# Performance work log

Measured on AMD Instinct MI355X. Metric: run time of the kernel, lower is better.

## Reference

```python
import jax, jax.numpy as jnp
import numpy as np

N_NODES, N_EDGES, NUM_GRAPHS = 50000, 800000, 64
F_DIM, H_DIM, N_LAYERS, N_CLASSES = 64, 64, 3, 16
EPS = 1e-5  # StdAggregation epsilon (PyG)


def setup_inputs() -> dict:
    key = jax.random.key(0)
    ks = jax.random.split(key, 12)
    s = 0.05
    x = jax.random.normal(ks[0], (N_NODES, F_DIM), jnp.float32)
    edge_index = jax.random.randint(ks[1], (2, N_EDGES), 0, N_NODES, dtype=jnp.int32)
    batch = jnp.sort(jax.random.randint(ks[2], (N_NODES,), 0, NUM_GRAPHS, dtype=jnp.int32))
    # per-layer PNAConv params (towers=1): pre Linear(2F->F), post Linear(13F->H), lin Linear(H->H)
    pre_w = jax.random.normal(ks[3], (N_LAYERS, F_DIM, 2 * F_DIM), jnp.float32) * s
    pre_b = jnp.zeros((N_LAYERS, F_DIM), jnp.float32)
    post_w = jax.random.normal(ks[4], (N_LAYERS, H_DIM, 13 * F_DIM), jnp.float32) * s
    post_b = jnp.zeros((N_LAYERS, H_DIM), jnp.float32)
    lin_w = jax.random.normal(ks[5], (N_LAYERS, H_DIM, H_DIM), jnp.float32) * s
    lin_b = jnp.zeros((N_LAYERS, H_DIM), jnp.float32)
    mlp_w1 = jax.random.normal(ks[6], (H_DIM, H_DIM), jnp.float32) * s
    mlp_b1 = jnp.zeros((H_DIM,), jnp.float32)
    mlp_w2 = jax.random.normal(ks[7], (N_CLASSES, H_DIM), jnp.float32) * s
    mlp_b2 = jnp.zeros((N_CLASSES,), jnp.float32)
    return dict(x=x, edge_index=edge_index, batch=batch,
                pre_w=pre_w, pre_b=pre_b, post_w=post_w, post_b=post_b,
                lin_w=lin_w, lin_b=lin_b, mlp_w1=mlp_w1, mlp_b1=mlp_b1,
                mlp_w2=mlp_w2, mlp_b2=mlp_b2)


def pna_forward(x, src, dst, pre_w, pre_b, post_w, post_b, lin_w, lin_b,
                mlp_w1, mlp_b1, mlp_w2, mlp_b2, batch):
    N = x.shape[0]
    deg_raw = jax.ops.segment_sum(jnp.ones_like(src, jnp.float32), dst, N)  # in-degree [N]
    deg = jnp.maximum(deg_raw, 1.0)[:, None]
    # avg log degree (PNA avg_deg['log'] from the degree histogram of this graph)
    avg_log = jnp.mean(jnp.log(deg_raw + 1.0))
    log_deg = jnp.log(deg + 1.0)
    amp = log_deg / avg_log          # amplification scaler [N,1]
    att = avg_log / log_deg          # attenuation scaler [N,1]
    has_in = (deg_raw > 0)[:, None]

    for l in range(pre_w.shape[0]):
        h = jnp.concatenate([x[dst], x[src]], axis=-1)        # [E, 2F] (x_i, x_j)
        m = h @ pre_w[l].T + pre_b[l]                          # pre_nn message [E, F]
        s1 = jax.ops.segment_sum(m, dst, N)
        s2 = jax.ops.segment_sum(m * m, dst, N)
        mean = s1 / deg
        std = jnp.sqrt(jax.nn.relu(s2 / deg - mean * mean) + EPS)
        mn = jnp.where(has_in, jax.ops.segment_min(m, dst, N), 0.0)
        mx = jnp.where(has_in, jax.ops.segment_max(m, dst, N), 0.0)
        aggr = jnp.concatenate([mean, mn, mx, std], axis=-1)   # [N, 4F]
        out = jnp.concatenate([x, aggr, aggr * amp, aggr * att], axis=-1)  # [N, 13F]
        out = out @ post_w[l].T + post_b[l]                    # post_nn [N, H]
        x = jax.nn.relu(out @ lin_w[l].T + lin_b[l])           # conv.lin + outer ReLU

    # global mean pool over graphs
    counts = jnp.maximum(
        jax.ops.segment_sum(jnp.ones((N,), x.dtype), batch, NUM_GRAPHS), 1.0)
    g = jax.ops.segment_sum(x, batch, NUM_GRAPHS) / counts[:, None]  # [G, H]
    g = jax.nn.relu(g @ mlp_w1.T + mlp_b1)
    return g @ mlp_w2.T + mlp_b2                               # [G, C]


def reference(x, edge_index, batch, pre_w, pre_b, post_w, post_b,
              lin_w, lin_b, mlp_w1, mlp_b1, mlp_w2, mlp_b2):
    src, dst = edge_index[0], edge_index[1]
    return pna_forward(x, src, dst, pre_w, pre_b, post_w, post_b,
                       lin_w, lin_b, mlp_w1, mlp_b1, mlp_w2, mlp_b2, batch)
```

## Files before the change

kernel.cpp:

```cpp
#include <hip/hip_runtime.h>
#include <math.h>

#define N_NODES   50000
#define N_EDGES   800000
#define NUM_GRAPHS 64
#define FDIM      64
#define HDIM      64
#define NLAYERS   3
#define NCLASSES  16
#define EPS       1e-5f

#define SCAN_CHUNK 1024
#define NCHUNKS ((N_NODES + SCAN_CHUNK - 1) / SCAN_CHUNK)

typedef unsigned short u16;
typedef unsigned int   u32;
typedef __attribute__((ext_vector_type(8))) short short8;
typedef __attribute__((ext_vector_type(4))) float floatx4;

#define WKS_LAYER 159744
#define PRES_LAYER 24576
#define KPOST_LDS_BYTES 106496

__device__ inline void split1(float f, u16& h, u16& m, u16& l) {
    u32 b  = __float_as_uint(f);
    u32 hb = b & 0xFFFF0000u;
    float r = f - __uint_as_float(hb);
    u32 mb = __float_as_uint(r) & 0xFFFF0000u;
    float r2 = r - __uint_as_float(mb);
    u32 lb = __float_as_uint(r2) & 0xFFFF0000u;
    h = (u16)(hb >> 16); m = (u16)(mb >> 16); l = (u16)(lb >> 16);
}

__device__ inline void gl_lds16(const void* g, void* l) {
    __builtin_amdgcn_global_load_lds(
        (const __attribute__((address_space(1))) u32*)g,
        (__attribute__((address_space(3))) u32*)l, 16, 0, 0);
}

__global__ __launch_bounds__(256) void k_comb(const float* __restrict__ post_w,
                                              const float* __restrict__ lin_w,
                                              const float* __restrict__ pre_w,
                                              const float* __restrict__ post_b,
                                              const float* __restrict__ lin_b,
                                              u16* __restrict__ WkS,
                                              u16* __restrict__ PreS,
                                              float* __restrict__ bcv,
                                              int* __restrict__ cnt,
                                              float* __restrict__ logsum) {
    int b = blockIdx.x, t = threadIdx.x;
    int zi = b * 256 + t;
    if (zi < N_NODES) cnt[zi] = 0;
    if (zi == 0) *logsum = 0.f;

    if (b < 624) {
        int c  = t & 63;
        int kl = t >> 6;
        int l  = b / 208;
        int o  = (b % 208) * 4 + kl;
        const float* lw = lin_w + (size_t)l * 4096 + c * 64;
        const float* pw = post_w + (size_t)l * 53248 + o;
        float acc = 0.f;
        #pragma unroll 8
        for (int j = 0; j < 64; ++j)
            acc += lw[j] * pw[(size_t)j * 832];
        u16 h, m, lo;
        split1(acc, h, m, lo);

        int kn;
        if (o < 64) kn = o;
        else {
            int s  = (o - 64) >> 8;
            int mm = (o - 64) & 255;
            int j  = mm >> 5, r = mm & 31;
            kn = 64 + j * 96 + s * 32 + r;
        }
        int ch  = kn >> 5;
        int kin = kn & 31;
        int n16 = c & 15, nt = c >> 4;
        int swk = (((kin >> 3) + (n16 >> 1)) & 3) * 8 + (kin & 7);
        size_t base = (size_t)l * WKS_LAYER + (size_t)ch * 6144
                    + nt * 512 + n16 * 32 + swk;
        WkS[base]        = h;
        WkS[base + 2048] = m;
        WkS[base + 4096] = lo;
    } else if (b == 624) {
        if (t < 192) {
            int l = t >> 6, c = t & 63;
            float acc = lin_b[l * 64 + c];
            for (int j = 0; j < 64; ++j)
                acc += lin_w[(size_t)l * 4096 + c * 64 + j] * post_b[l * 64 + j];
            bcv[l * 64 + c] = acc;
        }
    } else {
        int i = (b - 625) * 256 + t;
        int l = i >> 13;
        int rem = i & 8191;
        int c128 = rem >> 6;
        int k = rem & 63;
        float v;
        if (c128 < 64) v = pre_w[(size_t)l * 8192 + c128 * 128 + k];
        else           v = pre_w[(size_t)l * 8192 + (c128 - 64) * 128 + 64 + k];
        u16 h, m, lo;
        split1(v, h, m, lo);
        int ch = k >> 5, kin = k & 31;
        int nt = c128 >> 4, n16 = c128 & 15;
        int swk = (((kin >> 3) + (n16 >> 1)) & 3) * 8 + (kin & 7);
        size_t base = (size_t)l * PRES_LAYER + (size_t)ch * 12288
                    + nt * 512 + n16 * 32 + swk;
        PreS[base]        = h;
        PreS[base + 4096] = m;
        PreS[base + 8192] = lo;
    }
}

__global__ void k_count(const int* __restrict__ dst, int* __restrict__ cnt,
                        int* __restrict__ rank) {
    int e = blockIdx.x * 256 + threadIdx.x;
    if (e < N_EDGES) rank[e] = atomicAdd(&cnt[dst[e]], 1);
}

__global__ void k_chunk_sums(const int* __restrict__ cnt, int* __restrict__ bsum,
                             float* __restrict__ logsum) {
    __shared__ int   ired[256];
    __shared__ float lred[256];
    int b = blockIdx.x, t = threadIdx.x;
    int base = b * SCAN_CHUNK;
    int s = 0; float ls = 0.f;
    for (int i = t; i < SCAN_CHUNK; i += 256) {
        int idx = base + i;
        if (idx < N_NODES) {
            int v = cnt[idx];
            s += v;
            ls += logf((float)v + 1.0f);
        }
    }
    ired[t] = s; lred[t] = ls;
    __syncthreads();
    for (int off = 128; off > 0; off >>= 1) {
        if (t < off) { ired[t] += ired[t + off]; lred[t] += lred[t + off]; }
        __syncthreads();
    }
    if (t == 0) { bsum[b] = ired[0]; atomicAdd(logsum, lred[0]); }
}

__global__ void k_scan_top(const int* __restrict__ bsum, int* __restrict__ boff,
                           int* __restrict__ row_start) {
    if (threadIdx.x == 0) {
        int acc = 0;
        for (int i = 0; i < NCHUNKS; ++i) { boff[i] = acc; acc += bsum[i]; }
        row_start[N_NODES] = acc;
    }
}

__global__ void k_scan_chunks(const int* __restrict__ cnt, const int* __restrict__ boff,
                              int* __restrict__ row_start) {
    __shared__ int tsum[256];
    int b = blockIdx.x, t = threadIdx.x;
    int base = b * SCAN_CHUNK + t * 4;
    int v[4]; int s = 0;
    #pragma unroll
    for (int i = 0; i < 4; ++i) {
        int idx = base + i;
        v[i] = (idx < N_NODES) ? cnt[idx] : 0;
        s += v[i];
    }
    tsum[t] = s;
    __syncthreads();
    for (int off = 1; off < 256; off <<= 1) {
        int val = (t >= off) ? tsum[t - off] : 0;
        __syncthreads();
        tsum[t] += val;
        __syncthreads();
    }
    int excl = boff[b] + tsum[t] - s;
    #pragma unroll
    for (int i = 0; i < 4; ++i) {
        int idx = base + i;
        if (idx < N_NODES) row_start[idx] = excl;
        excl += v[i];
    }
}

__global__ void k_scatter(const int* __restrict__ src, const int* __restrict__ dst,
                          const int* __restrict__ rank,
                          const int* __restrict__ row_start,
                          int* __restrict__ csr_src) {
    int e = blockIdx.x * 256 + threadIdx.x;
    if (e < N_EDGES) {
        int d = dst[e];
        csr_src[row_start[d] + rank[e]] = src[e];
    }
}

__global__ void k_scal(const int* __restrict__ cnt, const float* __restrict__ logsum,
                       float* __restrict__ inv_deg, float* __restrict__ ampv,
                       float* __restrict__ attv, float* __restrict__ g_sum,
                       int* __restrict__ g_cnt) {
    int n = blockIdx.x * 256 + threadIdx.x;
    if (blockIdx.x == 0) {
        for (int i = threadIdx.x; i < 4096; i += 256) g_sum[i] = 0.f;
        if (threadIdx.x < 64) g_cnt[threadIdx.x] = 0;
    }
    if (n < N_NODES) {
        float avg = logsum[0] / (float)N_NODES;
        float degf = fmaxf((float)cnt[n], 1.0f);
        inv_deg[n] = 1.0f / degf;
        float ld = logf(degf + 1.0f);
        ampv[n] = ld / avg;
        attv[n] = avg / ld;
    }
}

__global__ __launch_bounds__(256, 4) void k_pre(const float* __restrict__ x,
                                                const u16* __restrict__ PreS,
                                                const float* __restrict__ pre_b,
                                                float* __restrict__ p,
                                                float* __restrict__ q) {
    __shared__ u16 ldsB[2 * 8192];
    int t = threadIdx.x;
    int w = t >> 6;
    int lane = t & 63;
    int m = lane & 15;
    int qh = lane >> 4;
    int rowBase = blockIdx.x * 64;

    int myrow = rowBase + 16 * w + m;
    bool vr = myrow < N_NODES;
    int crow = vr ? myrow : 0;
    const float* xrow = x + (size_t)crow * 64;

    int bo = m * 32 + ((qh + (m >> 1)) & 3) * 8;

    for (int u = w; u < 32; u += 4) {
        int ch = u >> 4, sp = (u >> 3) & 1, nt = u & 7;
        const char* g = (const char*)PreS + (size_t)ch * 24576 + sp * 8192
                      + nt * 1024 + lane * 16;
        char* l = (char*)ldsB + u * 1024;
        gl_lds16(g, l);
    }
    float fa[2][8];
    #pragma unroll
    for (int ch = 0; ch < 2; ++ch) {
        const float* sp = xrow + ch * 32 + qh * 8;
        float4 u0 = *(const float4*)sp;
        float4 u1 = *(const float4*)(sp + 4);
        fa[ch][0] = vr ? u0.x : 0.f; fa[ch][1] = vr ? u0.y : 0.f;
        fa[ch][2] = vr ? u0.z : 0.f; fa[ch][3] = vr ? u0.w : 0.f;
        fa[ch][4] = vr ? u1.x : 0.f; fa[ch][5] = vr ? u1.y : 0.f;
        fa[ch][6] = vr ? u1.z : 0.f; fa[ch][7] = vr ? u1.w : 0.f;
    }
    asm volatile("s_waitcnt vmcnt(0)" ::: "memory");
    __syncthreads();

    floatx4 acc[8] = {};
    #pragma unroll
    for (int ch = 0; ch < 2; ++ch) {
        union { u32 u[4]; short8 s8; } AH, AM;
        #pragma unroll
        for (int i = 0; i < 4; ++i) {
            float f0 = fa[ch][2 * i], f1 = fa[ch][2 * i + 1];
            u32 b0 = __float_as_uint(f0), b1 = __float_as_uint(f1);
            u32 h0 = b0 & 0xFFFF0000u,  h1 = b1 & 0xFFFF0000u;
            float r0 = f0 - __uint_as_float(h0);
            float r1 = f1 - __uint_as_float(h1);
            u32 m0 = __float_as_uint(r0) & 0xFFFF0000u;
            u32 m1 = __float_as_uint(r1) & 0xFFFF0000u;
            AH.u[i] = (h0 >> 16) | h1;
            AM.u[i] = (m0 >> 16) | m1;
        }
        const u16* Bb = ldsB + ch * 8192;
        #pragma unroll
        for (int nt = 0; nt < 8; ++nt) {
            short8 bH = *(const short8*)(Bb + nt * 512 + bo);
            short8 bM = *(const short8*)(Bb + 4096 + nt * 512 + bo);
            acc[nt] = __builtin_amdgcn_mfma_f32_16x16x32_bf16(AH.s8, bH, acc[nt], 0, 0, 0);
            acc[nt] = __builtin_amdgcn_mfma_f32_16x16x32_bf16(AH.s8, bM, acc[nt], 0, 0, 0);
            acc[nt] = __builtin_amdgcn_mfma_f32_16x16x32_bf16(AM.s8, bH, acc[nt], 0, 0, 0);
        }
    }

    int col = m;
    #pragma unroll
    for (int nt = 0; nt < 8; ++nt) {
        int cbase = (nt & 3) * 16 + col;
        float bias = (nt < 4) ? pre_b[cbase] : 0.f;
        float* outp = (nt < 4) ? p : q;
        #pragma unroll
        for (int reg = 0; reg < 4; ++reg) {
            int grow = rowBase + 16 * w + qh * 4 + reg;
            if (grow < N_NODES)
                outp[(size_t)grow * 64 + cbase] = acc[nt][reg] + bias;
        }
    }
}

__global__ __launch_bounds__(256) void k_aggr(const float* __restrict__ p,
                                              const float* __restrict__ q,
                                              const int* __restrict__ row_start,
                                              const int* __restrict__ csr_src,
                                              const float* __restrict__ inv_deg,
                                              float* __restrict__ aggr) {
    int wid  = (blockIdx.x * 256 + threadIdx.x) >> 6;
    int lane = threadIdx.x & 63;
    if (wid >= N_NODES) return;
    int n = wid;
    int beg = row_start[n], end = row_start[n + 1];
    float sum = 0.f, sq = 0.f;
    float mn = INFINITY, mx = -INFINITY;
    int e = beg;
    for (; e + 7 < end; e += 8) {
        float qv[8];
        #pragma unroll
        for (int u = 0; u < 8; ++u) {
            int s = csr_src[e + u];
            qv[u] = q[(size_t)s * 64 + lane];
        }
        #pragma unroll
        for (int u = 0; u < 8; ++u) {
            float m = qv[u];
            sum += m; sq += m * m;
            mn = fminf(mn, m); mx = fmaxf(mx, m);
        }
    }
    for (; e + 3 < end; e += 4) {
        float qv[4];
        #pragma unroll
        for (int u = 0; u < 4; ++u) {
            int s = csr_src[e + u];
            qv[u] = q[(size_t)s * 64 + lane];
        }
        #pragma unroll
        for (int u = 0; u < 4; ++u) {
            float m = qv[u];
            sum += m; sq += m * m;
            mn = fminf(mn, m); mx = fmaxf(mx, m);
        }
    }
    for (; e < end; ++e) {
        int s = csr_src[e];
        float m = q[(size_t)s * 64 + lane];
        sum += m; sq += m * m;
        mn = fminf(mn, m); mx = fmaxf(mx, m);
    }
    float* a = aggr + (size_t)n * 256;
    if (end <= beg) {
        a[lane]       = 0.f;
        a[64 + lane]  = 0.f;
        a[128 + lane] = 0.f;
        a[192 + lane] = sqrtf(EPS);
    } else {
        float pv = p[n * 64 + lane];
        float id = inv_deg[n];
        float meanq = sum * id;
        float var = fmaxf(sq * id - meanq * meanq, 0.f);
        a[lane]       = pv + meanq;
        a[64 + lane]  = pv + mn;
        a[128 + lane] = pv + mx;
        a[192 + lane] = sqrtf(var + EPS);
    }
}

__global__ __launch_bounds__(1024, 4) void k_post(const float* __restrict__ x,
                                                  const float* __restrict__ aggr,
                                                  const float* __restrict__ ampv,
                                                  const float* __restrict__ attv,
                                                  const u16* __restrict__ WkS,
                                                  const float* __restrict__ bc,
                                                  float* __restrict__ xout) {
    extern __shared__ u16 ldsB[];
    int t = threadIdx.x;
    int w = t >> 6;
    int lane = t & 63;
    int m = lane & 15;
    int qh = lane >> 4;

    int b  = blockIdx.x;
    int s8 = b & 7;
    int g  = b >> 3;
    int q2 = g >> 1;
    int nh = g & 1;
    int r  = 8 * q2 + s8;
    if (r >= 98) return;
    int rowBase = r * 512 + 32 * w;

    for (int u = w; u < 104; u += 16) {
        int ch = u >> 2;
        int sp = (u >> 1) & 1;
        int h2 = u & 1;
        const char* gp = (const char*)WkS + ch * 12288 + sp * 4096
                       + nh * 2048 + h2 * 1024 + lane * 16;
        char* l = (char*)ldsB + u * 1024;
        gl_lds16(gp, l);
    }

    int row0 = rowBase + m;
    int row1 = row0 + 16;
    int cr0 = (row0 < N_NODES) ? row0 : 0;
    int cr1 = (row1 < N_NODES) ? row1 : 0;
    const float* xr0 = x + (size_t)cr0 * 64;
    const float* xr1 = x + (size_t)cr1 * 64;
    const float* ar0 = aggr + (size_t)cr0 * 256;
    const float* ar1 = aggr + (size_t)cr1 * 256;

    int bo = m * 32 + ((qh + (m >> 1)) & 3) * 8;

    floatx4 accP0[2] = {}, accA0[2] = {}, accT0[2] = {};
    floatx4 accP1[2] = {}, accA1[2] = {}, accT1[2] = {};

    float f0[8], f1[8];
    union U8 { u32 u[4]; short8 s8v; };
    U8 AH0, AM0, AH1, AM1;

    auto loadRaw = [&](const float* sp, float* f) {
        float4 u0 = *(const float4*)(sp + qh * 8);
        float4 u1 = *(const float4*)(sp + qh * 8 + 4);
        f[0] = u0.x; f[1] = u0.y; f[2] = u0.z; f[3] = u0.w;
        f[4] = u1.x; f[5] = u1.y; f[6] = u1.z; f[7] = u1.w;
    };
    auto split2 = [&](const float* f, U8& H, U8& M8) {
        #pragma unroll
        for (int i = 0; i < 4; ++i) {
            float v0 = f[2 * i], v1 = f[2 * i + 1];
            u32 b0 = __float_as_uint(v0), b1 = __float_as_uint(v1);
            u32 h0 = b0 & 0xFFFF0000u,  h1 = b1 & 0xFFFF0000u;
            float r0 = v0 - __uint_as_float(h0);
            float r1 = v1 - __uint_as_float(h1);
            u32 m0 = __float_as_uint(r0) & 0xFFFF0000u;
            u32 m1 = __float_as_uint(r1) & 0xFFFF0000u;
            H.u[i]  = (h0 >> 16) | h1;
            M8.u[i] = (m0 >> 16) | m1;
        }
    };
    #define MF(A, B, C) C = __builtin_amdgcn_mfma_f32_16x16x32_bf16((A).s8v, (B), (C), 0, 0, 0)
    auto chunkMM = [&](int ch, floatx4* A0, floatx4* A1) {
        const u16* pB = ldsB + ch * 2048 + bo;
        short8 bH0 = *(const short8*)(pB);
        short8 bH1 = *(const short8*)(pB + 512);
        short8 bM0 = *(const short8*)(pB + 1024);
        short8 bM1 = *(const short8*)(pB + 1536);
        MF(AH0, bH0, A0[0]); MF(AH1, bH0, A1[0]); MF(AH0, bH1, A0[1]); MF(AH1, bH1, A1[1]);
        MF(AH0, bM0, A0[0]); MF(AH1, bM0, A1[0]); MF(AH0, bM1, A0[1]); MF(AH1, bM1, A1[1]);
        MF(AM0, bH0, A0[0]); MF(AM1, bH0, A1[0]); MF(AM0, bH1, A0[1]); MF(AM1, bH1, A1[1]);
    };

    loadRaw(xr0, f0); loadRaw(xr1, f1);
    asm volatile("s_waitcnt vmcnt(0)" ::: "memory");
    __syncthreads();

    split2(f0, AH0, AM0); split2(f1, AH1, AM1);
    loadRaw(xr0 + 32, f0); loadRaw(xr1 + 32, f1);
    chunkMM(0, accP0, accP1);
    split2(f0, AH0, AM0); split2(f1, AH1, AM1);
    loadRaw(ar0, f0); loadRaw(ar1, f1);
    chunkMM(1, accP0, accP1);
    for (int j = 0; j < 8; ++j) {
        split2(f0, AH0, AM0); split2(f1, AH1, AM1);
        if (j < 7) { loadRaw(ar0 + (j + 1) * 32, f0); loadRaw(ar1 + (j + 1) * 32, f1); }
        int ch = 2 + 3 * j;
        chunkMM(ch,     accP0, accP1);
        chunkMM(ch + 1, accA0, accA1);
        chunkMM(ch + 2, accT0, accT1);
    }
    #undef MF

    int col = m;
    #pragma unroll
    for (int frag = 0; frag < 2; ++frag) {
        #pragma unroll
        for (int reg = 0; reg < 4; ++reg) {
            int grow = rowBase + 16 * frag + qh * 4 + reg;
            if (grow < N_NODES) {
                float av = ampv[grow], tv = attv[grow];
                #pragma unroll
                for (int nt = 0; nt < 2; ++nt) {
                    int cbase = (nh * 2 + nt) * 16 + col;
                    float pv  = frag ? accP1[nt][reg] : accP0[nt][reg];
                    float av2 = frag ? accA1[nt][reg] : accA0[nt][reg];
                    float tv2 = frag ? accT1[nt][reg] : accT0[nt][reg];
                    float v = pv + av * av2 + tv * tv2 + bc[cbase];
                    xout[(size_t)grow * 64 + cbase] = fmaxf(v, 0.f);
                }
            }
        }
    }
}

__global__ __launch_bounds__(256) void k_pool(const float* __restrict__ x,
                                              const int* __restrict__ batch,
                                              float* __restrict__ g_sum,
                                              int* __restrict__ g_cnt) {
    int lane = threadIdx.x & 63;
    int wave = blockIdx.x * 4 + (threadIdx.x >> 6);
    const int NPW = 16;
    int beg = wave * NPW;
    if (beg >= N_NODES) return;
    int end = min(beg + NPW, N_NODES);
    float acc = 0.f;
    int cur = batch[beg];
    int c = 0;
    for (int n = beg; n < end; ++n) {
        int b = batch[n];
        if (b != cur) {
            atomicAdd(&g_sum[cur * 64 + lane], acc);
            if (lane == 0) atomicAdd(&g_cnt[cur], c);
            acc = 0.f; c = 0; cur = b;
        }
        acc += x[n * 64 + lane];
        ++c;
    }
    atomicAdd(&g_sum[cur * 64 + lane], acc);
    if (lane == 0) atomicAdd(&g_cnt[cur], c);
}

__global__ __launch_bounds__(256) void k_mlp(const float* __restrict__ g_sum,
                                             const int* __restrict__ g_cnt,
                                             const float* __restrict__ w1,
                                             const float* __restrict__ b1,
                                             const float* __restrict__ w2,
                                             const float* __restrict__ b2,
                                             float* __restrict__ out) {
    __shared__ float g[64][64];
    __shared__ float h[64][64];
    __shared__ float wT[64][65];
    int t = threadIdx.x;
    for (int idx = t; idx < 4096; idx += 256) {
        int gi = idx >> 6, c = idx & 63;
        float cntf = fmaxf((float)g_cnt[gi], 1.f);
        g[gi][c] = g_sum[idx] / cntf;
    }
    for (int idx = t; idx < 4096; idx += 256) {
        int c = idx >> 6, k = idx & 63;
        wT[k][c] = w1[c * 64 + k];
    }
    __syncthreads();
    for (int idx = t; idx < 4096; idx += 256) {
        int gi = idx >> 6, c = idx & 63;
        float acc = b1[c];
        for (int k = 0; k < 64; ++k) acc += g[gi][k] * wT[k][c];
        h[gi][c] = fmaxf(acc, 0.f);
    }
    __syncthreads();
    for (int idx = t; idx < 64 * NCLASSES; idx += 256) {
        int gi = idx >> 4, c = idx & 15;
        float acc = b2[c];
        for (int k = 0; k < 64; ++k) acc += h[gi][k] * w2[c * 64 + k];
        out[gi * NCLASSES + c] = acc;
    }
}

extern "C" void kernel_launch(void* const* d_in, const int* in_sizes, int n_in,
                              void* d_out, int out_size, void* d_ws, size_t ws_size,
                              hipStream_t stream) {
    const float* x      = (const float*)d_in[0];
    const int*   ei     = (const int*)d_in[1];
    const int*   batch  = (const int*)d_in[2];
    const float* pre_w  = (const float*)d_in[3];
    const float* pre_b  = (const float*)d_in[4];
    const float* post_w = (const float*)d_in[5];
    const float* post_b = (const float*)d_in[6];
    const float* lin_w  = (const float*)d_in[7];
    const float* lin_b  = (const float*)d_in[8];
    const float* mlp_w1 = (const float*)d_in[9];
    const float* mlp_b1 = (const float*)d_in[10];
    const float* mlp_w2 = (const float*)d_in[11];
    const float* mlp_b2 = (const float*)d_in[12];

    const int* src = ei;
    const int* dst = ei + N_EDGES;

    char* base = (char*)d_ws;
    size_t off = 0;
    auto alloc = [&](size_t bytes) -> void* {
        void* ptr = base + off;
        off += (bytes + 255) & ~(size_t)255;
        return ptr;
    };
    int*   cnt       = (int*)alloc(N_NODES * 4);
    int*   row_start = (int*)alloc((N_NODES + 1) * 4);
    int*   rank      = (int*)alloc(N_EDGES * 4);
    int*   csr_src   = (int*)alloc(N_EDGES * 4);
    int*   bsum      = (int*)alloc(64 * 4);
    int*   boff      = (int*)alloc(64 * 4);
    float* logsum    = (float*)alloc(16);
    float* inv_deg   = (float*)alloc(N_NODES * 4);
    float* ampv      = (float*)alloc(N_NODES * 4);
    float* attv      = (float*)alloc(N_NODES * 4);
    float* p         = (float*)alloc((size_t)N_NODES * 64 * 4);
    float* q         = (float*)alloc((size_t)N_NODES * 64 * 4);
    float* aggr      = (float*)alloc((size_t)N_NODES * 256 * 4);
    float* xb0       = (float*)alloc((size_t)N_NODES * 64 * 4);
    float* xb1       = (float*)alloc((size_t)N_NODES * 64 * 4);
    float* g_sum     = (float*)alloc(64 * 64 * 4);
    int*   g_cnt     = (int*)alloc(64 * 4);
    u16*   WkS       = (u16*)alloc((size_t)3 * WKS_LAYER * 2);
    u16*   PreS      = (u16*)alloc((size_t)3 * PRES_LAYER * 2);
    float* bcv       = (float*)alloc(3 * 64 * 4);

    k_comb<<<721, 256, 0, stream>>>(post_w, lin_w, pre_w, post_b, lin_b,
                                    WkS, PreS, bcv, cnt, logsum);

    k_count<<<(N_EDGES + 255) / 256, 256, 0, stream>>>(dst, cnt, rank);
    k_chunk_sums<<<NCHUNKS, 256, 0, stream>>>(cnt, bsum, logsum);
    k_scan_top<<<1, 64, 0, stream>>>(bsum, boff, row_start);
    k_scan_chunks<<<NCHUNKS, 256, 0, stream>>>(cnt, boff, row_start);
    k_scatter<<<(N_EDGES + 255) / 256, 256, 0, stream>>>(src, dst, rank,
                                                         row_start, csr_src);
    k_scal<<<(N_NODES + 255) / 256, 256, 0, stream>>>(cnt, logsum, inv_deg,
                                                      ampv, attv, g_sum, g_cnt);

    const int PRE_BLOCKS  = (N_NODES + 63) / 64;
    const int POST_BLOCKS = 208;
    const float* xin = x;
    float* bufs[3] = {xb0, xb1, xb0};
    for (int l = 0; l < NLAYERS; ++l) {
        k_pre<<<PRE_BLOCKS, 256, 0, stream>>>(xin, PreS + (size_t)l * PRES_LAYER,
                                              pre_b + l * 64, p, q);
        k_aggr<<<(N_NODES + 3) / 4, 256, 0, stream>>>(p, q, row_start, csr_src,
                                                      inv_deg, aggr);
        float* xo = bufs[l];
        k_post<<<POST_BLOCKS, 1024, KPOST_LDS_BYTES, stream>>>(
            xin, aggr, ampv, attv, WkS + (size_t)l * WKS_LAYER,
            bcv + l * 64, xo);
        xin = xo;
    }

    int pool_waves = (N_NODES + 15) / 16;
    k_pool<<<(pool_waves + 3) / 4, 256, 0, stream>>>(xin, batch, g_sum, g_cnt);
    k_mlp<<<1, 256, 0, stream>>>(g_sum, g_cnt, mlp_w1, mlp_b1, mlp_w2, mlp_b2,
                                 (float*)d_out);
}
```

Baseline: 408.2 us.

## Fuse degree scalars and scan top into scan kernel; fuse pooling into last post

```diff
diff --git a/kernel.cpp b/kernel.cpp
--- a/kernel.cpp
+++ b/kernel.cpp
@@ -47,11 +47,15 @@
                                               u16* __restrict__ PreS,
                                               float* __restrict__ bcv,
                                               int* __restrict__ cnt,
-                                              float* __restrict__ logsum) {
+                                              float* __restrict__ logsum,
+                                              float* __restrict__ g_sum,
+                                              int* __restrict__ g_cnt) {
     int b = blockIdx.x, t = threadIdx.x;
     int zi = b * 256 + t;
     if (zi < N_NODES) cnt[zi] = 0;
     if (zi == 0) *logsum = 0.f;
+    if (zi < 4096) g_sum[zi] = 0.f;
+    if (zi < 64)   g_cnt[zi] = 0;
 
     if (b < 624) {
         int c  = t & 63;
@@ -144,19 +148,21 @@
     if (t == 0) { bsum[b] = ired[0]; atomicAdd(logsum, lred[0]); }
 }
 
-__global__ void k_scan_top(const int* __restrict__ bsum, int* __restrict__ boff,
-                           int* __restrict__ row_start) {
-    if (threadIdx.x == 0) {
-        int acc = 0;
-        for (int i = 0; i < NCHUNKS; ++i) { boff[i] = acc; acc += bsum[i]; }
-        row_start[N_NODES] = acc;
-    }
-}
-
-__global__ void k_scan_chunks(const int* __restrict__ cnt, const int* __restrict__ boff,
-                              int* __restrict__ row_start) {
+__global__ __launch_bounds__(256) void k_scan2(const int* __restrict__ cnt,
+                                               const int* __restrict__ bsum,
+                                               const float* __restrict__ logsum,
+                                               const int* __restrict__ batch,
+                                               int* __restrict__ row_start,
+                                               float* __restrict__ inv_deg,
+                                               float* __restrict__ ampv,
+                                               float* __restrict__ attv,
+                                               int* __restrict__ g_cnt) {
     __shared__ int tsum[256];
     int b = blockIdx.x, t = threadIdx.x;
+
+    int boffb = 0;
+    for (int i = 0; i < b; ++i) boffb += bsum[i];
+
     int base = b * SCAN_CHUNK + t * 4;
     int v[4]; int s = 0;
     #pragma unroll
@@ -173,13 +179,31 @@
         tsum[t] += val;
         __syncthreads();
     }
-    int excl = boff[b] + tsum[t] - s;
+    int excl = boffb + tsum[t] - s;
+    float avg = logsum[0] / (float)N_NODES;
+
+    int curb = -1, c = 0;
     #pragma unroll
     for (int i = 0; i < 4; ++i) {
         int idx = base + i;
-        if (idx < N_NODES) row_start[idx] = excl;
-        excl += v[i];
-    }
+        if (idx < N_NODES) {
+            row_start[idx] = excl;
+            excl += v[i];
+            float degf = fmaxf((float)v[i], 1.0f);
+            inv_deg[idx] = 1.0f / degf;
+            float ld = logf(degf + 1.0f);
+            ampv[idx] = ld / avg;
+            attv[idx] = avg / ld;
+            int bb = batch[idx];
+            if (bb != curb) {
+                if (c) atomicAdd(&g_cnt[curb], c);
+                curb = bb; c = 0;
+            }
+            ++c;
+        }
+    }
+    if (c) atomicAdd(&g_cnt[curb], c);
+    if (b == 0 && t == 0) row_start[N_NODES] = N_EDGES;
 }
 
 __global__ void k_scatter(const int* __restrict__ src, const int* __restrict__ dst,
@@ -190,25 +214,6 @@
     if (e < N_EDGES) {
         int d = dst[e];
         csr_src[row_start[d] + rank[e]] = src[e];
-    }
-}
-
-__global__ void k_scal(const int* __restrict__ cnt, const float* __restrict__ logsum,
-                       float* __restrict__ inv_deg, float* __restrict__ ampv,
-                       float* __restrict__ attv, float* __restrict__ g_sum,
-                       int* __restrict__ g_cnt) {
-    int n = blockIdx.x * 256 + threadIdx.x;
-    if (blockIdx.x == 0) {
-        for (int i = threadIdx.x; i < 4096; i += 256) g_sum[i] = 0.f;
-        if (threadIdx.x < 64) g_cnt[threadIdx.x] = 0;
-    }
-    if (n < N_NODES) {
-        float avg = logsum[0] / (float)N_NODES;
-        float degf = fmaxf((float)cnt[n], 1.0f);
-        inv_deg[n] = 1.0f / degf;
-        float ld = logf(degf + 1.0f);
-        ampv[n] = ld / avg;
-        attv[n] = avg / ld;
     }
 }
 
@@ -367,7 +372,9 @@
                                                   const float* __restrict__ attv,
                                                   const u16* __restrict__ WkS,
                                                   const float* __restrict__ bc,
-                                                  float* __restrict__ xout) {
+                                                  float* __restrict__ xout,
+                                                  const int* __restrict__ batch,
+                                                  float* __restrict__ g_sum) {
     extern __shared__ u16 ldsB[];
     int t = threadIdx.x;
     int w = t >> 6;
@@ -465,52 +472,64 @@
     #undef MF
 
     int col = m;
-    #pragma unroll
-    for (int frag = 0; frag < 2; ++frag) {
-        #pragma unroll
-        for (int reg = 0; reg < 4; ++reg) {
-            int grow = rowBase + 16 * frag + qh * 4 + reg;
-            if (grow < N_NODES) {
-                float av = ampv[grow], tv = attv[grow];
-                #pragma unroll
-                for (int nt = 0; nt < 2; ++nt) {
-                    int cbase = (nh * 2 + nt) * 16 + col;
-                    float pv  = frag ? accP1[nt][reg] : accP0[nt][reg];
-                    float av2 = frag ? accA1[nt][reg] : accA0[nt][reg];
-                    float tv2 = frag ? accT1[nt][reg] : accT0[nt][reg];
-                    float v = pv + av * av2 + tv * tv2 + bc[cbase];
-                    xout[(size_t)grow * 64 + cbase] = fmaxf(v, 0.f);
+    int cb0 = (nh * 2 + 0) * 16 + col;
+    int cb1 = (nh * 2 + 1) * 16 + col;
+    if (batch == nullptr) {
+        #pragma unroll
+        for (int frag = 0; frag < 2; ++frag) {
+            #pragma unroll
+            for (int reg = 0; reg < 4; ++reg) {
+                int grow = rowBase + 16 * frag + qh * 4 + reg;
+                if (grow < N_NODES) {
+                    float av = ampv[grow], tv = attv[grow];
+                    #pragma unroll
+                    for (int nt = 0; nt < 2; ++nt) {
+                        int cbase = nt ? cb1 : cb0;
+                        float pv  = frag ? accP1[nt][reg] : accP0[nt][reg];
+                        float av2 = frag ? accA1[nt][reg] : accA0[nt][reg];
+                        float tv2 = frag ? accT1[nt][reg] : accT0[nt][reg];
+                        float v = pv + av * av2 + tv * tv2 + bc[cbase];
+                        xout[(size_t)grow * 64 + cbase] = fmaxf(v, 0.f);
+                    }
                 }
             }
         }
-    }
-}
-
-__global__ __launch_bounds__(256) void k_pool(const float* __restrict__ x,
-                                              const int* __restrict__ batch,
-                                              float* __restrict__ g_sum,
-                                              int* __restrict__ g_cnt) {
-    int lane = threadIdx.x & 63;
-    int wave = blockIdx.x * 4 + (threadIdx.x >> 6);
-    const int NPW = 16;
-    int beg = wave * NPW;
-    if (beg >= N_NODES) return;
-    int end = min(beg + NPW, N_NODES);
-    float acc = 0.f;
-    int cur = batch[beg];
-    int c = 0;
-    for (int n = beg; n < end; ++n) {
-        int b = batch[n];
-        if (b != cur) {
-            atomicAdd(&g_sum[cur * 64 + lane], acc);
-            if (lane == 0) atomicAdd(&g_cnt[cur], c);
-            acc = 0.f; c = 0; cur = b;
-        }
-        acc += x[n * 64 + lane];
-        ++c;
-    }
-    atomicAdd(&g_sum[cur * 64 + lane], acc);
-    if (lane == 0) atomicAdd(&g_cnt[cur], c);
+    } else {
+        float acc0 = 0.f, acc1 = 0.f;
+        int cur = -1;
+        float bias0 = bc[cb0], bias1 = bc[cb1];
+        #pragma unroll
+        for (int frag = 0; frag < 2; ++frag) {
+            #pragma unroll
+            for (int reg = 0; reg < 4; ++reg) {
+                int grow = rowBase + 16 * frag + qh * 4 + reg;
+                if (grow < N_NODES) {
+                    float av = ampv[grow], tv = attv[grow];
+                    float p0 = frag ? accP0[0][reg] * 0.f + accP1[0][reg] : accP0[0][reg];
+                    float a0 = frag ? accA1[0][reg] : accA0[0][reg];
+                    float t0 = frag ? accT1[0][reg] : accT0[0][reg];
+                    float p1 = frag ? accP1[1][reg] : accP0[1][reg];
+                    float a1 = frag ? accA1[1][reg] : accA0[1][reg];
+                    float t1 = frag ? accT1[1][reg] : accT0[1][reg];
+                    float v0 = fmaxf(p0 + av * a0 + tv * t0 + bias0, 0.f);
+                    float v1 = fmaxf(p1 + av * a1 + tv * t1 + bias1, 0.f);
+                    int bb = batch[grow];
+                    if (bb != cur) {
+                        if (cur >= 0) {
+                            atomicAdd(&g_sum[cur * 64 + cb0], acc0);
+                            atomicAdd(&g_sum[cur * 64 + cb1], acc1);
+                        }
+                        cur = bb; acc0 = 0.f; acc1 = 0.f;
+                    }
+                    acc0 += v0; acc1 += v1;
+                }
+            }
+        }
+        if (cur >= 0) {
+            atomicAdd(&g_sum[cur * 64 + cb0], acc0);
+            atomicAdd(&g_sum[cur * 64 + cb1], acc1);
+        }
+    }
 }
 
 __global__ __launch_bounds__(256) void k_mlp(const float* __restrict__ g_sum,
@@ -581,7 +600,6 @@
     int*   rank      = (int*)alloc(N_EDGES * 4);
     int*   csr_src   = (int*)alloc(N_EDGES * 4);
     int*   bsum      = (int*)alloc(64 * 4);
-    int*   boff      = (int*)alloc(64 * 4);
     float* logsum    = (float*)alloc(16);
     float* inv_deg   = (float*)alloc(N_NODES * 4);
     float* ampv      = (float*)alloc(N_NODES * 4);
@@ -598,16 +616,14 @@
     float* bcv       = (float*)alloc(3 * 64 * 4);
 
     k_comb<<<721, 256, 0, stream>>>(post_w, lin_w, pre_w, post_b, lin_b,
-                                    WkS, PreS, bcv, cnt, logsum);
+                                    WkS, PreS, bcv, cnt, logsum, g_sum, g_cnt);
 
     k_count<<<(N_EDGES + 255) / 256, 256, 0, stream>>>(dst, cnt, rank);
     k_chunk_sums<<<NCHUNKS, 256, 0, stream>>>(cnt, bsum, logsum);
-    k_scan_top<<<1, 64, 0, stream>>>(bsum, boff, row_start);
-    k_scan_chunks<<<NCHUNKS, 256, 0, stream>>>(cnt, boff, row_start);
+    k_scan2<<<NCHUNKS, 256, 0, stream>>>(cnt, bsum, logsum, batch, row_start,
+                                         inv_deg, ampv, attv, g_cnt);
     k_scatter<<<(N_EDGES + 255) / 256, 256, 0, stream>>>(src, dst, rank,
                                                          row_start, csr_src);
-    k_scal<<<(N_NODES + 255) / 256, 256, 0, stream>>>(cnt, logsum, inv_deg,
-                                                      ampv, attv, g_sum, g_cnt);
 
     const int PRE_BLOCKS  = (N_NODES + 63) / 64;
     const int POST_BLOCKS = 208;
@@ -619,14 +635,13 @@
         k_aggr<<<(N_NODES + 3) / 4, 256, 0, stream>>>(p, q, row_start, csr_src,
                                                       inv_deg, aggr);
         float* xo = bufs[l];
+        const int* bptr = (l == NLAYERS - 1) ? batch : nullptr;
         k_post<<<POST_BLOCKS, 1024, KPOST_LDS_BYTES, stream>>>(
             xin, aggr, ampv, attv, WkS + (size_t)l * WKS_LAYER,
-            bcv + l * 64, xo);
+            bcv + l * 64, xo, bptr, g_sum);
         xin = xo;
     }
 
-    int pool_waves = (N_NODES + 15) / 16;
-    k_pool<<<(pool_waves + 3) / 4, 256, 0, stream>>>(xin, batch, g_sum, g_cnt);
     k_mlp<<<1, 256, 0, stream>>>(g_sum, g_cnt, mlp_w1, mlp_b1, mlp_w2, mlp_b2,
                                  (float*)d_out);
 }
```

New measurement: 455.1 us. 11.5% more time.
